# Performance work log

Measured on AMD Instinct MI355X. Metric: run time of the kernel, lower is better.

Reference implementation:

```python
import jax, jax.numpy as jnp
import numpy as np

FEATURES = 1024
HEAD_DIM = 64
NUM_HEADS = 16
EPS = 1e-5


def setup_inputs() -> dict:
    key = jax.random.key(0)
    ks = jax.random.split(key, 6)
    x = jax.random.normal(ks[0], (2, 2048, FEATURES), dtype=jnp.float32)
    s_in = 1.0 / np.sqrt(FEATURES)
    s_hd = 1.0 / np.sqrt(NUM_HEADS * HEAD_DIM)
    return {
        "x": x,
        "gamma": jnp.ones((FEATURES,), jnp.float32),
        "beta": jnp.zeros((FEATURES,), jnp.float32),
        "Wq": jax.random.normal(ks[1], (FEATURES, NUM_HEADS * HEAD_DIM), jnp.float32) * s_in,
        "Wkv": jax.random.normal(ks[2], (FEATURES, 2 * HEAD_DIM), jnp.float32) * s_in,
        "Wo": jax.random.normal(ks[3], (NUM_HEADS * HEAD_DIM, FEATURES), jnp.float32) * s_hd,
        "bo": jax.random.normal(ks[4], (FEATURES,), jnp.float32) * s_hd,
    }


def reference(x, gamma, beta, Wq, Wkv, Wo, bo):
    # LayerNorm over last dim
    mu = jnp.mean(x, axis=-1, keepdims=True)
    var = jnp.mean(jnp.square(x - mu), axis=-1, keepdims=True)
    xn = (x - mu) * jax.lax.rsqrt(var + EPS) * gamma + beta

    b, t, _ = x.shape
    q = (xn @ Wq).reshape(b, t, NUM_HEADS, HEAD_DIM).transpose(0, 2, 1, 3)  # b h t d
    kv = xn @ Wkv  # b s 2d
    k, v = kv[..., :HEAD_DIM], kv[..., HEAD_DIM:]  # b s d (single shared head)

    scale = HEAD_DIM ** (-0.5)
    attn = jnp.einsum('bhtd,bsd->bhts', q, k) * scale
    attn = jax.nn.softmax(attn, axis=-1)
    out = jnp.einsum('bhts,bsd->bhtd', attn, v)
    out = out.transpose(0, 2, 1, 3).reshape(b, t, NUM_HEADS * HEAD_DIM)
    return out @ Wo + bo + x
```

## Files before the change

### kernel.cpp

```cpp
#include <hip/hip_runtime.h>

typedef __attribute__((ext_vector_type(8))) __bf16 bf16x8;
typedef __attribute__((ext_vector_type(4))) float floatx4;
typedef unsigned short u16;
typedef unsigned int u32;

#define KSCALE 0.18033688011112042f

__device__ __forceinline__ u16 f2bf(float f) {
    union { float f; u32 u; } v; v.f = f;
    u32 r = v.u + 0x7fffu + ((v.u >> 16) & 1u);
    return (u16)(r >> 16);
}

__device__ __forceinline__ u32 pk2bf(float a, float b) {
    union { float f; u32 u; } x, y; x.f = a; y.f = b;
    return __builtin_amdgcn_perm(y.u + 0x8000u, x.u + 0x8000u, 0x07060302);
}

__device__ __forceinline__ void gl_lds16(const u16* g, u16* l) {
    __builtin_amdgcn_global_load_lds((const __attribute__((address_space(1))) void*)g,
                                     (__attribute__((address_space(3))) void*)l, 16, 0, 0);
}

__global__ __launch_bounds__(256) void prep(const float* __restrict__ Wq, const float* __restrict__ Wkv,
                                            const float* __restrict__ Wo, const float* __restrict__ x,
                                            const float* __restrict__ gamma, const float* __restrict__ beta,
                                            u16* __restrict__ WqkvT, u16* __restrict__ WoT,
                                            u16* __restrict__ xn) {
    __shared__ float tile[64][68];
    __shared__ float ps[4], ps2[4];
    const int bx = blockIdx.x;
    const int t = threadIdx.x;
    if (bx < 768) {
        const int z = bx >> 8, rem = bx & 255;
        const int tr = (rem >> 4) * 64, tc = (rem & 15) * 64;
        const float* in = (z == 0) ? Wq : (z == 1 ? Wkv : Wo);
        u16* out = (z == 0) ? WqkvT : (z == 1 ? WqkvT + (size_t)1024 * 1024 : WoT);
        const int cols = (z == 1) ? 128 : 1024;
        if (tc >= cols) return;
        for (int p = 0; p < 4; p++) {
            int ri = (t >> 4) + p * 16;
            int ci = (t & 15) * 4;
            float4 v = *(const float4*)&in[(size_t)(tr + ri) * cols + tc + ci];
            tile[ri][ci + 0] = v.x; tile[ri][ci + 1] = v.y;
            tile[ri][ci + 2] = v.z; tile[ri][ci + 3] = v.w;
        }
        __syncthreads();
        for (int p = 0; p < 4; p++) {
            int oc = (t >> 4) + p * 16;
            int ir = (t & 15) * 4;
            float s = (z == 1 && (tc + oc) < 64) ? KSCALE : 1.0f;
            ushort4 o;
            o.x = f2bf(tile[ir + 0][oc] * s);
            o.y = f2bf(tile[ir + 1][oc] * s);
            o.z = f2bf(tile[ir + 2][oc] * s);
            o.w = f2bf(tile[ir + 3][oc] * s);
            *(ushort4*)&out[(size_t)(tc + oc) * 1024 + tr + ir] = o;
        }
    } else {
        const int row = bx - 768;
        const float* xr = x + (size_t)row * 1024;
        float4 v = *(const float4*)&xr[t * 4];
        float s = v.x + v.y + v.z + v.w;
        float s2 = v.x * v.x + v.y * v.y + v.z * v.z + v.w * v.w;
        for (int off = 1; off < 64; off <<= 1) {
            s += __shfl_xor(s, off, 64);
            s2 += __shfl_xor(s2, off, 64);
        }
        int w = t >> 6, lane = t & 63;
        if (lane == 0) { ps[w] = s; ps2[w] = s2; }
        __syncthreads();
        float S = ps[0] + ps[1] + ps[2] + ps[3];
        float S2 = ps2[0] + ps2[1] + ps2[2] + ps2[3];
        float mu = S * (1.0f / 1024.0f);
        float var = S2 * (1.0f / 1024.0f) - mu * mu;
        float rstd = rsqrtf(var + 1e-5f);
        ushort4 o;
        o.x = f2bf((v.x - mu) * rstd * gamma[t * 4 + 0] + beta[t * 4 + 0]);
        o.y = f2bf((v.y - mu) * rstd * gamma[t * 4 + 1] + beta[t * 4 + 1]);
        o.z = f2bf((v.z - mu) * rstd * gamma[t * 4 + 2] + beta[t * 4 + 2]);
        o.w = f2bf((v.w - mu) * rstd * gamma[t * 4 + 3] + beta[t * 4 + 3]);
        *(ushort4*)&xn[(size_t)row * 1024 + t * 4] = o;
    }
}

template <bool FINAL>
__global__ __launch_bounds__(256) void gemm_bt(const u16* __restrict__ A, const u16* __restrict__ BT,
                                               u16* __restrict__ Cb, float* __restrict__ Cf,
                                               const float* __restrict__ bias, const float* __restrict__ resid,
                                               u16* __restrict__ vt2, int M, int N, int K) {
    __shared__ u16 as_[64 * 64];
    __shared__ u16 bs_[128 * 64];
    const int t = threadIdx.x;
    const int w = t >> 6, lane = t & 63, q = lane >> 4, c = lane & 15;
    const int tm = blockIdx.y * 64, tn = blockIdx.x * 128;
    const int wm = (w & 1) * 32, wn = (w >> 1) * 64;

    const int l3 = lane >> 3, sch = lane & 7;
    const int arow = w * 16 + l3;
    const int aswz = (sch ^ (arow & 7)) * 8;
    const int brow = w * 32 + l3;
    const int bswz = (sch ^ (brow & 7)) * 8;
    const u16* ag0 = A + (size_t)(tm + arow) * K + aswz;
    const u16* ag1 = ag0 + (size_t)8 * K;
    const u16* bg0 = BT + (size_t)(tn + brow) * K + bswz;
    const u16* bg1 = bg0 + (size_t)8 * K;
    const u16* bg2 = bg0 + (size_t)16 * K;
    const u16* bg3 = bg0 + (size_t)24 * K;
    u16* al0 = as_ + (w * 16) * 64;
    u16* al1 = as_ + (w * 16 + 8) * 64;
    u16* bl0 = bs_ + (w * 32) * 64;
    u16* bl1 = bs_ + (w * 32 + 8) * 64;
    u16* bl2 = bs_ + (w * 32 + 16) * 64;
    u16* bl3 = bs_ + (w * 32 + 24) * 64;

    floatx4 acc[2][4];
    for (int i = 0; i < 2; i++)
        for (int j = 0; j < 4; j++) acc[i][j] = (floatx4){0.f, 0.f, 0.f, 0.f};

    const int c7 = c & 7;
    for (int k0 = 0; k0 < K; k0 += 64) {
        __syncthreads();
        gl_lds16(ag0 + k0, al0);
        gl_lds16(ag1 + k0, al1);
        gl_lds16(bg0 + k0, bl0);
        gl_lds16(bg1 + k0, bl1);
        gl_lds16(bg2 + k0, bl2);
        gl_lds16(bg3 + k0, bl3);
        __syncthreads();
        bf16x8 af[2][2], bf[4][2];
#pragma unroll
        for (int i = 0; i < 2; i++)
#pragma unroll
            for (int kk = 0; kk < 2; kk++)
                af[i][kk] = *(const bf16x8*)&as_[(wm + i * 16 + c) * 64 + (((kk * 4 + q) ^ c7) * 8)];
#pragma unroll
        for (int j = 0; j < 4; j++)
#pragma unroll
            for (int kk = 0; kk < 2; kk++)
                bf[j][kk] = *(const bf16x8*)&bs_[(wn + j * 16 + c) * 64 + (((kk * 4 + q) ^ c7) * 8)];
#pragma unroll
        for (int kk = 0; kk < 2; kk++)
#pragma unroll
            for (int i = 0; i < 2; i++)
#pragma unroll
                for (int j = 0; j < 4; j++)
                    acc[i][j] = __builtin_amdgcn_mfma_f32_16x16x32_bf16(af[i][kk], bf[j][kk], acc[i][j], 0, 0, 0);
    }
#pragma unroll
    for (int i = 0; i < 2; i++)
#pragma unroll
        for (int j = 0; j < 4; j++)
#pragma unroll
            for (int r = 0; r < 4; r++) {
                int row = tm + wm + i * 16 + q * 4 + r;
                int col = tn + wn + j * 16 + c;
                float v = acc[i][j][r];
                if (FINAL) {
                    Cf[(size_t)row * N + col] = v + bias[col] + resid[(size_t)row * N + col];
                } else if (col < 1088) {
                    Cb[(size_t)row * N + col] = f2bf(v);
                } else {
                    int d = col - 1088;
                    int bb = row >> 11, sl = row & 2047;
                    int Bk = sl >> 5, u = sl & 31;
                    int up = ((u >> 2) & 3) * 8 + ((u >> 4) << 2) + (u & 3);
                    vt2[((size_t)(bb * 64 + d)) * 2048 + Bk * 32 + up] = f2bf(v);
                }
            }
}

union Vf { bf16x8 v; u32 w[4]; };

__global__ __launch_bounds__(256, 2) void attn9(const u16* __restrict__ qkv, const u16* __restrict__ vt2,
                                                u16* __restrict__ out) {
    __shared__ u16 ksm[2][64 * 64];
    __shared__ u16 vsm[2][64 * 64];
    const int t = threadIdx.x;
    const int w = t >> 6, lane = t & 63;
    const int q = lane >> 4, c = lane & 15;
    const int qt = blockIdx.x, hg = blockIdx.y, b = blockIdx.z;
    const int h = hg * 4 + w;
    const size_t qrow0 = (size_t)b * 2048 + qt * 32;
    const u16* kbase = qkv + (size_t)b * 2048 * 1152 + 1024;
    const u16* vbase = vt2 + (size_t)b * 64 * 2048;

    const int l3 = lane >> 3, sch = lane & 7;
    const int srow = w * 16 + l3;
    const int swz = (sch ^ (srow & 7)) * 8;
    const u16* kg0 = kbase + (size_t)srow * 1152 + swz;
    const u16* kg1 = kg0 + (size_t)8 * 1152;
    const u16* vg0 = vbase + (size_t)srow * 2048 + swz;
    const u16* vg1 = vg0 + (size_t)8 * 2048;
    u16* kl0 = &ksm[0][(w * 16) * 64];
    u16* kl1 = &ksm[0][(w * 16 + 8) * 64];
    u16* vl0 = &vsm[0][(w * 16) * 64];
    u16* vl1 = &vsm[0][(w * 16 + 8) * 64];

    const int c7 = c & 7;
    const u16* kfp[4][2];
    const u16* vfp[4][2];
#pragma unroll
    for (int ni = 0; ni < 4; ni++)
#pragma unroll
        for (int kk = 0; kk < 2; kk++) {
            kfp[ni][kk] = &ksm[0][(ni * 16 + c) * 64 + (((kk * 4 + q) ^ c7) * 8)];
            vfp[ni][kk] = &vsm[0][(ni * 16 + c) * 64 + (((kk * 4 + q) ^ c7) * 8)];
        }

    bf16x8 qf[2][2];
#pragma unroll
    for (int mi = 0; mi < 2; mi++)
#pragma unroll
        for (int kk = 0; kk < 2; kk++)
            qf[mi][kk] = *(const bf16x8*)&qkv[(qrow0 + mi * 16 + c) * 1152 + h * 64 + kk * 32 + q * 8];

    floatx4 O[4][2], Lacc[2];
#pragma unroll
    for (int di = 0; di < 4; di++)
#pragma unroll
        for (int mi = 0; mi < 2; mi++) O[di][mi] = (floatx4){0.f, 0.f, 0.f, 0.f};
    Lacc[0] = (floatx4){0.f, 0.f, 0.f, 0.f};
    Lacc[1] = (floatx4){0.f, 0.f, 0.f, 0.f};
    Vf ones;
    ones.w[0] = ones.w[1] = ones.w[2] = ones.w[3] = 0x3F803F80u;

    gl_lds16(kg0, kl0);
    gl_lds16(kg1, kl1);
    gl_lds16(vg0, vl0);
    gl_lds16(vg1, vl1);
    kg0 += (size_t)64 * 1152; kg1 += (size_t)64 * 1152; vg0 += 64; vg1 += 64;
    __syncthreads();

#pragma unroll 2
    for (int tt = 0; tt < 32; tt++) {
        const int cur = tt & 1, nxt = cur ^ 1;
        if (tt < 31) {
            gl_lds16(kg0, kl0 + nxt * 4096);
            gl_lds16(kg1, kl1 + nxt * 4096);
            gl_lds16(vg0, vl0 + nxt * 4096);
            gl_lds16(vg1, vl1 + nxt * 4096);
            kg0 += (size_t)64 * 1152; kg1 += (size_t)64 * 1152; vg0 += 64; vg1 += 64;
        }

        bf16x8 kf[4][2];
        Vf vf[4][2];
#pragma unroll
        for (int ni = 0; ni < 4; ni++)
#pragma unroll
            for (int kk = 0; kk < 2; kk++)
                kf[ni][kk] = *(const bf16x8*)(kfp[ni][kk] + cur * 4096);
#pragma unroll
        for (int di = 0; di < 4; di++)
#pragma unroll
            for (int kk = 0; kk < 2; kk++)
                vf[di][kk].v = *(const bf16x8*)(vfp[di][kk] + cur * 4096);

        floatx4 sacc[4][2];
#pragma unroll
        for (int ni = 0; ni < 4; ni++)
#pragma unroll
            for (int mi = 0; mi < 2; mi++) {
                floatx4 z = (floatx4){0.f, 0.f, 0.f, 0.f};
                z = __builtin_amdgcn_mfma_f32_16x16x32_bf16(kf[ni][0], qf[mi][0], z, 0, 0, 0);
                z = __builtin_amdgcn_mfma_f32_16x16x32_bf16(kf[ni][1], qf[mi][1], z, 0, 0, 0);
                sacc[ni][mi] = z;
            }

        u32 pk[4][2][2];
#pragma unroll
        for (int mi = 0; mi < 2; mi++)
#pragma unroll
            for (int ni = 0; ni < 4; ni++) {
                float p0 = __builtin_amdgcn_exp2f(sacc[ni][mi][0]);
                float p1 = __builtin_amdgcn_exp2f(sacc[ni][mi][1]);
                float p2 = __builtin_amdgcn_exp2f(sacc[ni][mi][2]);
                float p3 = __builtin_amdgcn_exp2f(sacc[ni][mi][3]);
                pk[ni][mi][0] = pk2bf(p0, p1);
                pk[ni][mi][1] = pk2bf(p2, p3);
            }

#pragma unroll
        for (int kk = 0; kk < 2; kk++) {
            Vf pf[2];
#pragma unroll
            for (int mi = 0; mi < 2; mi++) {
                pf[mi].w[0] = pk[2 * kk][mi][0];
                pf[mi].w[1] = pk[2 * kk][mi][1];
                pf[mi].w[2] = pk[2 * kk + 1][mi][0];
                pf[mi].w[3] = pk[2 * kk + 1][mi][1];
            }
#pragma unroll
            for (int di = 0; di < 4; di++)
#pragma unroll
                for (int mi = 0; mi < 2; mi++)
                    O[di][mi] = __builtin_amdgcn_mfma_f32_16x16x32_bf16(vf[di][kk].v, pf[mi].v, O[di][mi], 0, 0, 0);
#pragma unroll
            for (int mi = 0; mi < 2; mi++)
                Lacc[mi] = __builtin_amdgcn_mfma_f32_16x16x32_bf16(ones.v, pf[mi].v, Lacc[mi], 0, 0, 0);
        }

        __syncthreads();
    }

    float inv[2] = {1.0f / Lacc[0][0], 1.0f / Lacc[1][0]};
#pragma unroll
    for (int di = 0; di < 4; di++)
#pragma unroll
        for (int mi = 0; mi < 2; mi++) {
            ushort4 o;
            o.x = f2bf(O[di][mi][0] * inv[mi]);
            o.y = f2bf(O[di][mi][1] * inv[mi]);
            o.z = f2bf(O[di][mi][2] * inv[mi]);
            o.w = f2bf(O[di][mi][3] * inv[mi]);
            *(ushort4*)&out[(qrow0 + mi * 16 + c) * 1024 + h * 64 + di * 16 + q * 4] = o;
        }
}

extern "C" void kernel_launch(void* const* d_in, const int* in_sizes, int n_in,
                              void* d_out, int out_size, void* d_ws, size_t ws_size,
                              hipStream_t stream) {
    const float* x = (const float*)d_in[0];
    const float* gamma = (const float*)d_in[1];
    const float* beta = (const float*)d_in[2];
    const float* Wq = (const float*)d_in[3];
    const float* Wkv = (const float*)d_in[4];
    const float* Wo = (const float*)d_in[5];
    const float* bo = (const float*)d_in[6];
    float* out = (float*)d_out;

    u16* WqkvT = (u16*)d_ws;
    u16* WoT = WqkvT + (size_t)1152 * 1024;
    u16* xn = WoT + (size_t)1024 * 1024;
    u16* qkv = xn + (size_t)4096 * 1024;
    u16* vt2 = qkv + (size_t)4096 * 1152;
    u16* attnO = xn;

    prep<<<4864, 256, 0, stream>>>(Wq, Wkv, Wo, x, gamma, beta, WqkvT, WoT, xn);
    gemm_bt<false><<<dim3(9, 64), 256, 0, stream>>>(xn, WqkvT, qkv, nullptr, nullptr, nullptr, vt2,
                                                    4096, 1152, 1024);
    attn9<<<dim3(64, 4, 2), 256, 0, stream>>>(qkv, vt2, attnO);
    gemm_bt<true><<<dim3(8, 64), 256, 0, stream>>>(attnO, WoT, nullptr, out, bo, x, nullptr,
                                                   4096, 1024, 1024);
}
```

Before: 165.3 us.

## Double-buffer GEMM LDS tiles and halve attention query tile per block

```diff
diff --git a/kernel.cpp b/kernel.cpp
--- a/kernel.cpp
+++ b/kernel.cpp
@@ -90,8 +90,8 @@
                                                u16* __restrict__ Cb, float* __restrict__ Cf,
                                                const float* __restrict__ bias, const float* __restrict__ resid,
                                                u16* __restrict__ vt2, int M, int N, int K) {
-    __shared__ u16 as_[64 * 64];
-    __shared__ u16 bs_[128 * 64];
+    __shared__ u16 as_[2 * 64 * 64];
+    __shared__ u16 bs_[2 * 128 * 64];
     const int t = threadIdx.x;
     const int w = t >> 6, lane = t & 63, q = lane >> 4, c = lane & 15;
     const int tm = blockIdx.y * 64, tn = blockIdx.x * 128;
@@ -115,31 +115,56 @@
     u16* bl2 = bs_ + (w * 32 + 16) * 64;
     u16* bl3 = bs_ + (w * 32 + 24) * 64;
 
+    const int c7 = c & 7;
+    const u16* afp[2][2];
+    const u16* bfp[4][2];
+#pragma unroll
+    for (int i = 0; i < 2; i++)
+#pragma unroll
+        for (int kk = 0; kk < 2; kk++)
+            afp[i][kk] = &as_[(wm + i * 16 + c) * 64 + (((kk * 4 + q) ^ c7) * 8)];
+#pragma unroll
+    for (int j = 0; j < 4; j++)
+#pragma unroll
+        for (int kk = 0; kk < 2; kk++)
+            bfp[j][kk] = &bs_[(wn + j * 16 + c) * 64 + (((kk * 4 + q) ^ c7) * 8)];
+
     floatx4 acc[2][4];
     for (int i = 0; i < 2; i++)
         for (int j = 0; j < 4; j++) acc[i][j] = (floatx4){0.f, 0.f, 0.f, 0.f};
 
-    const int c7 = c & 7;
-    for (int k0 = 0; k0 < K; k0 += 64) {
-        __syncthreads();
-        gl_lds16(ag0 + k0, al0);
-        gl_lds16(ag1 + k0, al1);
-        gl_lds16(bg0 + k0, bl0);
-        gl_lds16(bg1 + k0, bl1);
-        gl_lds16(bg2 + k0, bl2);
-        gl_lds16(bg3 + k0, bl3);
-        __syncthreads();
+    gl_lds16(ag0, al0);
+    gl_lds16(ag1, al1);
+    gl_lds16(bg0, bl0);
+    gl_lds16(bg1, bl1);
+    gl_lds16(bg2, bl2);
+    gl_lds16(bg3, bl3);
+    __syncthreads();
+
+    const int NIT = K >> 6;
+#pragma unroll 2
+    for (int it = 0; it < NIT; it++) {
+        const int cur = it & 1, nxt = cur ^ 1;
+        if (it + 1 < NIT) {
+            const int k0 = (it + 1) << 6;
+            gl_lds16(ag0 + k0, al0 + nxt * 4096);
+            gl_lds16(ag1 + k0, al1 + nxt * 4096);
+            gl_lds16(bg0 + k0, bl0 + nxt * 8192);
+            gl_lds16(bg1 + k0, bl1 + nxt * 8192);
+            gl_lds16(bg2 + k0, bl2 + nxt * 8192);
+            gl_lds16(bg3 + k0, bl3 + nxt * 8192);
+        }
         bf16x8 af[2][2], bf[4][2];
 #pragma unroll
         for (int i = 0; i < 2; i++)
 #pragma unroll
             for (int kk = 0; kk < 2; kk++)
-                af[i][kk] = *(const bf16x8*)&as_[(wm + i * 16 + c) * 64 + (((kk * 4 + q) ^ c7) * 8)];
+                af[i][kk] = *(const bf16x8*)(afp[i][kk] + cur * 4096);
 #pragma unroll
         for (int j = 0; j < 4; j++)
 #pragma unroll
             for (int kk = 0; kk < 2; kk++)
-                bf[j][kk] = *(const bf16x8*)&bs_[(wn + j * 16 + c) * 64 + (((kk * 4 + q) ^ c7) * 8)];
+                bf[j][kk] = *(const bf16x8*)(bfp[j][kk] + cur * 8192);
 #pragma unroll
         for (int kk = 0; kk < 2; kk++)
 #pragma unroll
@@ -147,6 +172,7 @@
 #pragma unroll
                 for (int j = 0; j < 4; j++)
                     acc[i][j] = __builtin_amdgcn_mfma_f32_16x16x32_bf16(af[i][kk], bf[j][kk], acc[i][j], 0, 0, 0);
+        __syncthreads();
     }
 #pragma unroll
     for (int i = 0; i < 2; i++)
@@ -173,8 +199,8 @@
 
 union Vf { bf16x8 v; u32 w[4]; };
 
-__global__ __launch_bounds__(256, 2) void attn9(const u16* __restrict__ qkv, const u16* __restrict__ vt2,
-                                                u16* __restrict__ out) {
+__global__ __launch_bounds__(256, 4) void attn10(const u16* __restrict__ qkv, const u16* __restrict__ vt2,
+                                                 u16* __restrict__ out) {
     __shared__ u16 ksm[2][64 * 64];
     __shared__ u16 vsm[2][64 * 64];
     const int t = threadIdx.x;
@@ -182,7 +208,7 @@
     const int q = lane >> 4, c = lane & 15;
     const int qt = blockIdx.x, hg = blockIdx.y, b = blockIdx.z;
     const int h = hg * 4 + w;
-    const size_t qrow0 = (size_t)b * 2048 + qt * 32;
+    const size_t qrow0 = (size_t)b * 2048 + qt * 16;
     const u16* kbase = qkv + (size_t)b * 2048 * 1152 + 1024;
     const u16* vbase = vt2 + (size_t)b * 64 * 2048;
 
@@ -209,20 +235,15 @@
             vfp[ni][kk] = &vsm[0][(ni * 16 + c) * 64 + (((kk * 4 + q) ^ c7) * 8)];
         }
 
-    bf16x8 qf[2][2];
-#pragma unroll
-    for (int mi = 0; mi < 2; mi++)
-#pragma unroll
-        for (int kk = 0; kk < 2; kk++)
-            qf[mi][kk] = *(const bf16x8*)&qkv[(qrow0 + mi * 16 + c) * 1152 + h * 64 + kk * 32 + q * 8];
-
-    floatx4 O[4][2], Lacc[2];
-#pragma unroll
-    for (int di = 0; di < 4; di++)
-#pragma unroll
-        for (int mi = 0; mi < 2; mi++) O[di][mi] = (floatx4){0.f, 0.f, 0.f, 0.f};
-    Lacc[0] = (floatx4){0.f, 0.f, 0.f, 0.f};
-    Lacc[1] = (floatx4){0.f, 0.f, 0.f, 0.f};
+    bf16x8 qf[2];
+#pragma unroll
+    for (int kk = 0; kk < 2; kk++)
+        qf[kk] = *(const bf16x8*)&qkv[(qrow0 + c) * 1152 + h * 64 + kk * 32 + q * 8];
+
+    floatx4 O[4], Lacc;
+#pragma unroll
+    for (int di = 0; di < 4; di++) O[di] = (floatx4){0.f, 0.f, 0.f, 0.f};
+    Lacc = (floatx4){0.f, 0.f, 0.f, 0.f};
     Vf ones;
     ones.w[0] = ones.w[1] = ones.w[2] = ones.w[3] = 0x3F803F80u;
 
@@ -257,65 +278,52 @@
             for (int kk = 0; kk < 2; kk++)
                 vf[di][kk].v = *(const bf16x8*)(vfp[di][kk] + cur * 4096);
 
-        floatx4 sacc[4][2];
-#pragma unroll
-        for (int ni = 0; ni < 4; ni++)
-#pragma unroll
-            for (int mi = 0; mi < 2; mi++) {
-                floatx4 z = (floatx4){0.f, 0.f, 0.f, 0.f};
-                z = __builtin_amdgcn_mfma_f32_16x16x32_bf16(kf[ni][0], qf[mi][0], z, 0, 0, 0);
-                z = __builtin_amdgcn_mfma_f32_16x16x32_bf16(kf[ni][1], qf[mi][1], z, 0, 0, 0);
-                sacc[ni][mi] = z;
-            }
-
-        u32 pk[4][2][2];
-#pragma unroll
-        for (int mi = 0; mi < 2; mi++)
-#pragma unroll
-            for (int ni = 0; ni < 4; ni++) {
-                float p0 = __builtin_amdgcn_exp2f(sacc[ni][mi][0]);
-                float p1 = __builtin_amdgcn_exp2f(sacc[ni][mi][1]);
-                float p2 = __builtin_amdgcn_exp2f(sacc[ni][mi][2]);
-                float p3 = __builtin_amdgcn_exp2f(sacc[ni][mi][3]);
-                pk[ni][mi][0] = pk2bf(p0, p1);
-                pk[ni][mi][1] = pk2bf(p2, p3);
-            }
+        floatx4 sacc[4];
+#pragma unroll
+        for (int ni = 0; ni < 4; ni++) {
+            floatx4 z = (floatx4){0.f, 0.f, 0.f, 0.f};
+            z = __builtin_amdgcn_mfma_f32_16x16x32_bf16(kf[ni][0], qf[0], z, 0, 0, 0);
+            z = __builtin_amdgcn_mfma_f32_16x16x32_bf16(kf[ni][1], qf[1], z, 0, 0, 0);
+            sacc[ni] = z;
+        }
+
+        u32 pk[4][2];
+#pragma unroll
+        for (int ni = 0; ni < 4; ni++) {
+            float p0 = __builtin_amdgcn_exp2f(sacc[ni][0]);
+            float p1 = __builtin_amdgcn_exp2f(sacc[ni][1]);
+            float p2 = __builtin_amdgcn_exp2f(sacc[ni][2]);
+            float p3 = __builtin_amdgcn_exp2f(sacc[ni][3]);
+            pk[ni][0] = pk2bf(p0, p1);
+            pk[ni][1] = pk2bf(p2, p3);
+        }
 
 #pragma unroll
         for (int kk = 0; kk < 2; kk++) {
-            Vf pf[2];
-#pragma unroll
-            for (int mi = 0; mi < 2; mi++) {
-                pf[mi].w[0] = pk[2 * kk][mi][0];
-                pf[mi].w[1] = pk[2 * kk][mi][1];
-                pf[mi].w[2] = pk[2 * kk + 1][mi][0];
-                pf[mi].w[3] = pk[2 * kk + 1][mi][1];
-            }
+            Vf pf;
+            pf.w[0] = pk[2 * kk][0];
+            pf.w[1] = pk[2 * kk][1];
+            pf.w[2] = pk[2 * kk + 1][0];
+            pf.w[3] = pk[2 * kk + 1][1];
 #pragma unroll
             for (int di = 0; di < 4; di++)
-#pragma unroll
-                for (int mi = 0; mi < 2; mi++)
-                    O[di][mi] = __builtin_amdgcn_mfma_f32_16x16x32_bf16(vf[di][kk].v, pf[mi].v, O[di][mi], 0, 0, 0);
-#pragma unroll
-            for (int mi = 0; mi < 2; mi++)
-                Lacc[mi] = __builtin_amdgcn_mfma_f32_16x16x32_bf16(ones.v, pf[mi].v, Lacc[mi], 0, 0, 0);
+                O[di] = __builtin_amdgcn_mfma_f32_16x16x32_bf16(vf[di][kk].v, pf.v, O[di], 0, 0, 0);
+            Lacc = __builtin_amdgcn_mfma_f32_16x16x32_bf16(ones.v, pf.v, Lacc, 0, 0, 0);
         }
 
         __syncthreads();
     }
 
-    float inv[2] = {1.0f / Lacc[0][0], 1.0f / Lacc[1][0]};
-#pragma unroll
-    for (int di = 0; di < 4; di++)
-#pragma unroll
-        for (int mi = 0; mi < 2; mi++) {
-            ushort4 o;
-            o.x = f2bf(O[di][mi][0] * inv[mi]);
-            o.y = f2bf(O[di][mi][1] * inv[mi]);
-            o.z = f2bf(O[di][mi][2] * inv[mi]);
-            o.w = f2bf(O[di][mi][3] * inv[mi]);
-            *(ushort4*)&out[(qrow0 + mi * 16 + c) * 1024 + h * 64 + di * 16 + q * 4] = o;
-        }
+    float inv = 1.0f / Lacc[0];
+#pragma unroll
+    for (int di = 0; di < 4; di++) {
+        ushort4 o;
+        o.x = f2bf(O[di][0] * inv);
+        o.y = f2bf(O[di][1] * inv);
+        o.z = f2bf(O[di][2] * inv);
+        o.w = f2bf(O[di][3] * inv);
+        *(ushort4*)&out[(qrow0 + c) * 1024 + h * 64 + di * 16 + q * 4] = o;
+    }
 }
 
 extern "C" void kernel_launch(void* const* d_in, const int* in_sizes, int n_in,
@@ -340,7 +348,7 @@
     prep<<<4864, 256, 0, stream>>>(Wq, Wkv, Wo, x, gamma, beta, WqkvT, WoT, xn);
     gemm_bt<false><<<dim3(9, 64), 256, 0, stream>>>(xn, WqkvT, qkv, nullptr, nullptr, nullptr, vt2,
                                                     4096, 1152, 1024);
-    attn9<<<dim3(64, 4, 2), 256, 0, stream>>>(qkv, vt2, attnO);
+    attn10<<<dim3(128, 4, 2), 256, 0, stream>>>(qkv, vt2, attnO);
     gemm_bt<true><<<dim3(8, 64), 256, 0, stream>>>(attnO, WoT, nullptr, out, bo, x, nullptr,
                                                    4096, 1024, 1024);
 }
```

New measurement: 167.8 us. About the same (+1.5%).

## Split attention over KV halves with combine kernel; double-buffer GEMM LDS loads

Applied to the files above, without the earlier changes.

```diff
diff --git a/kernel.cpp b/kernel.cpp
--- a/kernel.cpp
+++ b/kernel.cpp
@@ -90,8 +90,8 @@
                                                u16* __restrict__ Cb, float* __restrict__ Cf,
                                                const float* __restrict__ bias, const float* __restrict__ resid,
                                                u16* __restrict__ vt2, int M, int N, int K) {
-    __shared__ u16 as_[64 * 64];
-    __shared__ u16 bs_[128 * 64];
+    __shared__ u16 as_[2 * 64 * 64];
+    __shared__ u16 bs_[2 * 128 * 64];
     const int t = threadIdx.x;
     const int w = t >> 6, lane = t & 63, q = lane >> 4, c = lane & 15;
     const int tm = blockIdx.y * 64, tn = blockIdx.x * 128;
@@ -115,31 +115,56 @@
     u16* bl2 = bs_ + (w * 32 + 16) * 64;
     u16* bl3 = bs_ + (w * 32 + 24) * 64;
 
+    const int c7 = c & 7;
+    const u16* afp[2][2];
+    const u16* bfp[4][2];
+#pragma unroll
+    for (int i = 0; i < 2; i++)
+#pragma unroll
+        for (int kk = 0; kk < 2; kk++)
+            afp[i][kk] = &as_[(wm + i * 16 + c) * 64 + (((kk * 4 + q) ^ c7) * 8)];
+#pragma unroll
+    for (int j = 0; j < 4; j++)
+#pragma unroll
+        for (int kk = 0; kk < 2; kk++)
+            bfp[j][kk] = &bs_[(wn + j * 16 + c) * 64 + (((kk * 4 + q) ^ c7) * 8)];
+
     floatx4 acc[2][4];
     for (int i = 0; i < 2; i++)
         for (int j = 0; j < 4; j++) acc[i][j] = (floatx4){0.f, 0.f, 0.f, 0.f};
 
-    const int c7 = c & 7;
-    for (int k0 = 0; k0 < K; k0 += 64) {
-        __syncthreads();
-        gl_lds16(ag0 + k0, al0);
-        gl_lds16(ag1 + k0, al1);
-        gl_lds16(bg0 + k0, bl0);
-        gl_lds16(bg1 + k0, bl1);
-        gl_lds16(bg2 + k0, bl2);
-        gl_lds16(bg3 + k0, bl3);
-        __syncthreads();
+    gl_lds16(ag0, al0);
+    gl_lds16(ag1, al1);
+    gl_lds16(bg0, bl0);
+    gl_lds16(bg1, bl1);
+    gl_lds16(bg2, bl2);
+    gl_lds16(bg3, bl3);
+    __syncthreads();
+
+    const int NIT = K >> 6;
+#pragma unroll 2
+    for (int it = 0; it < NIT; it++) {
+        const int cur = it & 1, nxt = cur ^ 1;
+        if (it + 1 < NIT) {
+            const int k0 = (it + 1) << 6;
+            gl_lds16(ag0 + k0, al0 + nxt * 4096);
+            gl_lds16(ag1 + k0, al1 + nxt * 4096);
+            gl_lds16(bg0 + k0, bl0 + nxt * 8192);
+            gl_lds16(bg1 + k0, bl1 + nxt * 8192);
+            gl_lds16(bg2 + k0, bl2 + nxt * 8192);
+            gl_lds16(bg3 + k0, bl3 + nxt * 8192);
+        }
         bf16x8 af[2][2], bf[4][2];
 #pragma unroll
         for (int i = 0; i < 2; i++)
 #pragma unroll
             for (int kk = 0; kk < 2; kk++)
-                af[i][kk] = *(const bf16x8*)&as_[(wm + i * 16 + c) * 64 + (((kk * 4 + q) ^ c7) * 8)];
+                af[i][kk] = *(const bf16x8*)(afp[i][kk] + cur * 4096);
 #pragma unroll
         for (int j = 0; j < 4; j++)
 #pragma unroll
             for (int kk = 0; kk < 2; kk++)
-                bf[j][kk] = *(const bf16x8*)&bs_[(wn + j * 16 + c) * 64 + (((kk * 4 + q) ^ c7) * 8)];
+                bf[j][kk] = *(const bf16x8*)(bfp[j][kk] + cur * 8192);
 #pragma unroll
         for (int kk = 0; kk < 2; kk++)
 #pragma unroll
@@ -147,6 +172,7 @@
 #pragma unroll
                 for (int j = 0; j < 4; j++)
                     acc[i][j] = __builtin_amdgcn_mfma_f32_16x16x32_bf16(af[i][kk], bf[j][kk], acc[i][j], 0, 0, 0);
+        __syncthreads();
     }
 #pragma unroll
     for (int i = 0; i < 2; i++)
@@ -173,18 +199,19 @@
 
 union Vf { bf16x8 v; u32 w[4]; };
 
-__global__ __launch_bounds__(256, 2) void attn9(const u16* __restrict__ qkv, const u16* __restrict__ vt2,
-                                                u16* __restrict__ out) {
+__global__ __launch_bounds__(256, 4) void attn11(const u16* __restrict__ qkv, const u16* __restrict__ vt2,
+                                                 float* __restrict__ Opart, float* __restrict__ Lpart) {
     __shared__ u16 ksm[2][64 * 64];
     __shared__ u16 vsm[2][64 * 64];
     const int t = threadIdx.x;
     const int w = t >> 6, lane = t & 63;
     const int q = lane >> 4, c = lane & 15;
-    const int qt = blockIdx.x, hg = blockIdx.y, b = blockIdx.z;
+    const int qt = blockIdx.x, hg = blockIdx.y;
+    const int zz = blockIdx.z, b = zz >> 1, sh = zz & 1;
     const int h = hg * 4 + w;
     const size_t qrow0 = (size_t)b * 2048 + qt * 32;
-    const u16* kbase = qkv + (size_t)b * 2048 * 1152 + 1024;
-    const u16* vbase = vt2 + (size_t)b * 64 * 2048;
+    const u16* kbase = qkv + (size_t)b * 2048 * 1152 + 1024 + (size_t)(sh * 1024) * 1152;
+    const u16* vbase = vt2 + (size_t)b * 64 * 2048 + sh * 1024;
 
     const int l3 = lane >> 3, sch = lane & 7;
     const int srow = w * 16 + l3;
@@ -234,9 +261,9 @@
     __syncthreads();
 
 #pragma unroll 2
-    for (int tt = 0; tt < 32; tt++) {
+    for (int tt = 0; tt < 16; tt++) {
         const int cur = tt & 1, nxt = cur ^ 1;
-        if (tt < 31) {
+        if (tt < 15) {
             gl_lds16(kg0, kl0 + nxt * 4096);
             gl_lds16(kg1, kl1 + nxt * 4096);
             gl_lds16(vg0, vl0 + nxt * 4096);
@@ -304,18 +331,34 @@
         __syncthreads();
     }
 
-    float inv[2] = {1.0f / Lacc[0][0], 1.0f / Lacc[1][0]};
+    float* Op = Opart + (size_t)sh * 4096 * 1024;
 #pragma unroll
     for (int di = 0; di < 4; di++)
 #pragma unroll
-        for (int mi = 0; mi < 2; mi++) {
-            ushort4 o;
-            o.x = f2bf(O[di][mi][0] * inv[mi]);
-            o.y = f2bf(O[di][mi][1] * inv[mi]);
-            o.z = f2bf(O[di][mi][2] * inv[mi]);
-            o.w = f2bf(O[di][mi][3] * inv[mi]);
-            *(ushort4*)&out[(qrow0 + mi * 16 + c) * 1024 + h * 64 + di * 16 + q * 4] = o;
-        }
+        for (int mi = 0; mi < 2; mi++)
+            *(floatx4*)&Op[(qrow0 + mi * 16 + c) * 1024 + h * 64 + di * 16 + q * 4] = O[di][mi];
+    if (q == 0) {
+#pragma unroll
+        for (int mi = 0; mi < 2; mi++)
+            Lpart[((size_t)sh * 4096 + qrow0 + mi * 16 + c) * 16 + h] = Lacc[mi][0];
+    }
+}
+
+__global__ __launch_bounds__(256) void combine(const float* __restrict__ Opart, const float* __restrict__ Lpart,
+                                               u16* __restrict__ attnO) {
+    const int row = blockIdx.x, t = threadIdx.x;
+    const int col = t * 4;
+    float4 o0 = *(const float4*)&Opart[(size_t)row * 1024 + col];
+    float4 o1 = *(const float4*)&Opart[(size_t)(4096 + row) * 1024 + col];
+    const int hh = col >> 6;
+    float L = Lpart[(size_t)row * 16 + hh] + Lpart[(size_t)(4096 + row) * 16 + hh];
+    float inv = 1.0f / L;
+    ushort4 o;
+    o.x = f2bf((o0.x + o1.x) * inv);
+    o.y = f2bf((o0.y + o1.y) * inv);
+    o.z = f2bf((o0.z + o1.z) * inv);
+    o.w = f2bf((o0.w + o1.w) * inv);
+    *(ushort4*)&attnO[(size_t)row * 1024 + col] = o;
 }
 
 extern "C" void kernel_launch(void* const* d_in, const int* in_sizes, int n_in,
@@ -335,12 +378,15 @@
     u16* xn = WoT + (size_t)1024 * 1024;
     u16* qkv = xn + (size_t)4096 * 1024;
     u16* vt2 = qkv + (size_t)4096 * 1152;
+    float* Opart = (float*)(vt2 + (size_t)2 * 64 * 2048);
+    float* Lpart = Opart + (size_t)2 * 4096 * 1024;
     u16* attnO = xn;
 
     prep<<<4864, 256, 0, stream>>>(Wq, Wkv, Wo, x, gamma, beta, WqkvT, WoT, xn);
     gemm_bt<false><<<dim3(9, 64), 256, 0, stream>>>(xn, WqkvT, qkv, nullptr, nullptr, nullptr, vt2,
                                                     4096, 1152, 1024);
-    attn9<<<dim3(64, 4, 2), 256, 0, stream>>>(qkv, vt2, attnO);
+    attn11<<<dim3(64, 4, 4), 256, 0, stream>>>(qkv, vt2, Opart, Lpart);
+    combine<<<4096, 256, 0, stream>>>(Opart, Lpart, attnO);
     gemm_bt<true><<<dim3(8, 64), 256, 0, stream>>>(attnO, WoT, nullptr, out, bo, x, nullptr,
                                                    4096, 1024, 1024);
 }
```

Measured after the change: 174.8 us. 5.7% more time.

## Double-buffer LDS tiles in the bf16 GEMM to overlap loads with MFMA

Applied to the files above, without the earlier changes.

```diff
diff --git a/kernel.cpp b/kernel.cpp
--- a/kernel.cpp
+++ b/kernel.cpp
@@ -90,8 +90,8 @@
                                                u16* __restrict__ Cb, float* __restrict__ Cf,
                                                const float* __restrict__ bias, const float* __restrict__ resid,
                                                u16* __restrict__ vt2, int M, int N, int K) {
-    __shared__ u16 as_[64 * 64];
-    __shared__ u16 bs_[128 * 64];
+    __shared__ u16 as_[2 * 64 * 64];
+    __shared__ u16 bs_[2 * 128 * 64];
     const int t = threadIdx.x;
     const int w = t >> 6, lane = t & 63, q = lane >> 4, c = lane & 15;
     const int tm = blockIdx.y * 64, tn = blockIdx.x * 128;
@@ -115,31 +115,56 @@
     u16* bl2 = bs_ + (w * 32 + 16) * 64;
     u16* bl3 = bs_ + (w * 32 + 24) * 64;
 
+    const int c7 = c & 7;
+    const u16* afp[2][2];
+    const u16* bfp[4][2];
+#pragma unroll
+    for (int i = 0; i < 2; i++)
+#pragma unroll
+        for (int kk = 0; kk < 2; kk++)
+            afp[i][kk] = &as_[(wm + i * 16 + c) * 64 + (((kk * 4 + q) ^ c7) * 8)];
+#pragma unroll
+    for (int j = 0; j < 4; j++)
+#pragma unroll
+        for (int kk = 0; kk < 2; kk++)
+            bfp[j][kk] = &bs_[(wn + j * 16 + c) * 64 + (((kk * 4 + q) ^ c7) * 8)];
+
     floatx4 acc[2][4];
     for (int i = 0; i < 2; i++)
         for (int j = 0; j < 4; j++) acc[i][j] = (floatx4){0.f, 0.f, 0.f, 0.f};
 
-    const int c7 = c & 7;
-    for (int k0 = 0; k0 < K; k0 += 64) {
-        __syncthreads();
-        gl_lds16(ag0 + k0, al0);
-        gl_lds16(ag1 + k0, al1);
-        gl_lds16(bg0 + k0, bl0);
-        gl_lds16(bg1 + k0, bl1);
-        gl_lds16(bg2 + k0, bl2);
-        gl_lds16(bg3 + k0, bl3);
-        __syncthreads();
+    gl_lds16(ag0, al0);
+    gl_lds16(ag1, al1);
+    gl_lds16(bg0, bl0);
+    gl_lds16(bg1, bl1);
+    gl_lds16(bg2, bl2);
+    gl_lds16(bg3, bl3);
+    __syncthreads();
+
+    const int NIT = K >> 6;
+#pragma unroll 2
+    for (int it = 0; it < NIT; it++) {
+        const int cur = it & 1, nxt = cur ^ 1;
+        if (it + 1 < NIT) {
+            const int k0 = (it + 1) << 6;
+            gl_lds16(ag0 + k0, al0 + nxt * 4096);
+            gl_lds16(ag1 + k0, al1 + nxt * 4096);
+            gl_lds16(bg0 + k0, bl0 + nxt * 8192);
+            gl_lds16(bg1 + k0, bl1 + nxt * 8192);
+            gl_lds16(bg2 + k0, bl2 + nxt * 8192);
+            gl_lds16(bg3 + k0, bl3 + nxt * 8192);
+        }
         bf16x8 af[2][2], bf[4][2];
 #pragma unroll
         for (int i = 0; i < 2; i++)
 #pragma unroll
             for (int kk = 0; kk < 2; kk++)
-                af[i][kk] = *(const bf16x8*)&as_[(wm + i * 16 + c) * 64 + (((kk * 4 + q) ^ c7) * 8)];
+                af[i][kk] = *(const bf16x8*)(afp[i][kk] + cur * 4096);
 #pragma unroll
         for (int j = 0; j < 4; j++)
 #pragma unroll
             for (int kk = 0; kk < 2; kk++)
-                bf[j][kk] = *(const bf16x8*)&bs_[(wn + j * 16 + c) * 64 + (((kk * 4 + q) ^ c7) * 8)];
+                bf[j][kk] = *(const bf16x8*)(bfp[j][kk] + cur * 8192);
 #pragma unroll
         for (int kk = 0; kk < 2; kk++)
 #pragma unroll
@@ -147,6 +172,7 @@
 #pragma unroll
                 for (int j = 0; j < 4; j++)
                     acc[i][j] = __builtin_amdgcn_mfma_f32_16x16x32_bf16(af[i][kk], bf[j][kk], acc[i][j], 0, 0, 0);
+        __syncthreads();
     }
 #pragma unroll
     for (int i = 0; i < 2; i++)
```

Measured after the change: 165.4 us, median of 2. About the same (+0.0%).
